# Performance work log

Hardware: AMD Instinct MI355X
Metric: run time of the kernel (lower is better)

The kernel has to match this reference:

```python
import jax, jax.numpy as jnp
import numpy as np

N = 100000   # total nodes
E = 1000000  # edges
D = 64       # input_dim
H = 128      # embed_dim


def setup_inputs() -> dict:
    key = jax.random.key(0)
    k1, k2, k3, k4 = jax.random.split(key, 4)
    nodes = jnp.arange(N, dtype=jnp.int32)
    features = jax.random.normal(k1, (N, D), dtype=jnp.float32)
    edge_index = jax.random.randint(k2, (2, E), 0, N, dtype=jnp.int32)
    # nn.Linear(2*D, H): weight [H, 2D], bias [H]
    W = jax.random.normal(k3, (H, 2 * D), dtype=jnp.float32) / np.sqrt(2 * D)
    b = jax.random.normal(k4, (H,), dtype=jnp.float32) * 0.01
    return {"nodes": nodes, "features": features, "edge_index": edge_index,
            "W": W, "b": b}


def reference(nodes, features, edge_index, W, b):
    src, dst = edge_index[0], edge_index[1]
    # gcn=False: neighbors are undirected (both src->dst and dst->src).
    # Mean aggregator over all neighbors (full-neighborhood mean).
    ones = jnp.ones((E,), dtype=features.dtype)
    neigh_sum = (jax.ops.segment_sum(features[dst], src, num_segments=N)
                 + jax.ops.segment_sum(features[src], dst, num_segments=N))
    deg = (jax.ops.segment_sum(ones, src, num_segments=N)
           + jax.ops.segment_sum(ones, dst, num_segments=N))
    neigh_mean = neigh_sum / jnp.maximum(deg, 1.0)[:, None]  # [N, D]
    self_feats = features[nodes]            # [B, D]
    neigh_feats = neigh_mean[nodes]         # [B, D]
    combined = jnp.concatenate([self_feats, neigh_feats], axis=1)  # [B, 2D]
    out = jax.nn.relu(combined @ W.T + b)   # [B, H]
    return out
```

## Files before the change

### kernel.cpp

```cpp
#include <hip/hip_runtime.h>
#include <hip/hip_bf16.h>


#define D_IN 64
#define H_OUT 128
#define CAP 64
#define CAP_L 61
#define NPB 32
#define BSHIFT 8
#define BUK_N 256
#define NBUK_MAX 512
#define PASSA_BLOCKS 256
#define PASSA_THREADS 512
#define OVF_CAP 32768

typedef unsigned long long ull;
typedef unsigned short ushortt;
typedef unsigned char uchar;
typedef __attribute__((ext_vector_type(8))) short bf16x8;
typedef __attribute__((ext_vector_type(4))) float f32x4;
typedef __attribute__((ext_vector_type(2))) float f32x2;

__device__ __forceinline__ ushortt f2bf(float f) {
    __hip_bfloat16 h = __float2bfloat16(f);
    return *reinterpret_cast<ushortt*>(&h);
}
__device__ __forceinline__ float bf2f(ushortt u) {
    unsigned int x = ((unsigned int)u) << 16;
    return __uint_as_float(x);
}

__global__ __launch_bounds__(PASSA_THREADS) void bucket_a_kernel(
    const int* __restrict__ ei,
    unsigned* __restrict__ gbuf,
    int* __restrict__ blkcnt,
    ull* __restrict__ ovf,
    int* __restrict__ ovfn,
    int E, int nbuk, int scap, int chunk)
{
    __shared__ int lcnt[NBUK_MAX];
    const int t = threadIdx.x;
    for (int i = t; i < nbuk; i += PASSA_THREADS) lcnt[i] = 0;
    __syncthreads();

    const int E2 = 2 * E;
    int lo = blockIdx.x * chunk;
    int hi = lo + chunk; if (hi > E2) hi = E2;

    for (int i = lo + t; i < hi; i += PASSA_THREADS) {
        int u = ei[i];
        int v = (i < E) ? ei[E + i] : ei[i - E];
        int b = u >> BSHIFT;
        unsigned pk = ((unsigned)v << BSHIFT) | (unsigned)(u & (BUK_N - 1));
        int p = atomicAdd(&lcnt[b], 1);
        if (p < scap) {
            gbuf[((size_t)blockIdx.x * nbuk + b) * scap + p] = pk;
        } else {
            int gp = atomicAdd(ovfn, 1);
            if (gp < OVF_CAP) ovf[gp] = ((ull)(unsigned)v << 32) | (unsigned)u;
        }
    }
    __syncthreads();
    for (int b = t; b < nbuk; b += PASSA_THREADS) {
        int c = lcnt[b];
        blkcnt[blockIdx.x * nbuk + b] = c < scap ? c : scap;
    }
}

__global__ __launch_bounds__(512) void adj_lds_kernel(
    const unsigned* __restrict__ gbuf,
    const int* __restrict__ blkcnt,
    const ull* __restrict__ ovf,
    const int* __restrict__ ovfn,
    int* __restrict__ cnt,
    int* __restrict__ adj,
    int N, int nbuk, int scap)
{
    __shared__ unsigned adj_l[BUK_N * CAP_L];
    __shared__ int cnt_l[BUK_N];
    __shared__ int scnt_l[PASSA_BLOCKS];

    const int b = blockIdx.x;
    const int t = threadIdx.x;

    if (t < BUK_N) cnt_l[t] = 0;
    if (t < PASSA_BLOCKS) scnt_l[t] = blkcnt[t * nbuk + b];
    __syncthreads();

    const int wv   = t >> 6;
    const int lane = t & 63;

    for (int seg = wv; seg < PASSA_BLOCKS; seg += 8) {
        int c = scnt_l[seg];
        const unsigned* base = gbuf + ((size_t)seg * nbuk + b) * scap;
        for (int i = lane; i < c; i += 64) {
            unsigned e = base[i];
            int ul = e & (BUK_N - 1);
            int v  = (int)(e >> BSHIFT);
            int p  = atomicAdd(&cnt_l[ul], 1);
            if (p < CAP_L) adj_l[ul * CAP_L + p] = (unsigned)v;
        }
    }
    __syncthreads();

    int novf = *ovfn; if (novf > OVF_CAP) novf = OVF_CAP;
    for (int i = t; i < novf; i += 512) {
        ull pk = ovf[i];
        int u = (int)(unsigned)(pk & 0xffffffffu);
        if ((u >> BSHIFT) == b) {
            int v = (int)(unsigned)(pk >> 32);
            int ul = u & (BUK_N - 1);
            int p  = atomicAdd(&cnt_l[ul], 1);
            if (p < CAP_L) adj_l[ul * CAP_L + p] = (unsigned)v;
        }
    }
    __syncthreads();

    if (t < BUK_N) {
        int g = (b << BSHIFT) + t;
        if (g < N) {
            int c = cnt_l[t];
            cnt[g] = c;
            int cl = c < CAP_L ? c : CAP_L;
            int k4 = (cl + 3) >> 2;
            for (int s = 0; s < k4; ++s) {
                uint4 o;
                o.x = adj_l[t * CAP_L + 4 * s + 0];
                o.y = adj_l[t * CAP_L + 4 * s + 1];
                o.z = adj_l[t * CAP_L + 4 * s + 2];
                o.w = adj_l[t * CAP_L + 4 * s + 3];
                *(uint4*)&adj[(size_t)g * CAP + 4 * s] = o;
            }
        }
    }
}

__global__ __launch_bounds__(256) void build_adj_kernel(
    const int* __restrict__ ei,
    int* __restrict__ cnt,
    int* __restrict__ adj,
    int E)
{
    const int part   = blockIdx.x & 7;
    const int bloc   = blockIdx.x >> 3;
    const int nbp    = gridDim.x >> 3;
    const int stride = nbp * 256;
    const int E2     = 2 * E;

    for (int i = bloc * 256 + (int)threadIdx.x; i < E2; i += stride) {
        int u = ei[i];
        if (((u >> 4) & 7) != part) continue;
        int v = (i < E) ? ei[E + i] : ei[i - E];
        int p = atomicAdd(&cnt[u], 1);
        if (p < CAP_L) adj[u * CAP + p] = v;
    }
}

__global__ __launch_bounds__(256) void convert_kernel(
    const float4* __restrict__ feat4,
    const float4* __restrict__ w4,
    ushortt* __restrict__ fb,
    uint2* __restrict__ fq,
    ushortt* __restrict__ Wb,
    int* __restrict__ ovfn,
    int nfeat8, int nw8)
{
    if (blockIdx.x == 0 && threadIdx.x == 0) *ovfn = 0;
    int i = blockIdx.x * 256 + threadIdx.x;
    if (i < nfeat8) {
        float4 a = feat4[2 * i], b = feat4[2 * i + 1];
        bf16x8 o;
        o[0] = (short)f2bf(a.x); o[1] = (short)f2bf(a.y);
        o[2] = (short)f2bf(a.z); o[3] = (short)f2bf(a.w);
        o[4] = (short)f2bf(b.x); o[5] = (short)f2bf(b.y);
        o[6] = (short)f2bf(b.z); o[7] = (short)f2bf(b.w);
        *(bf16x8*)&fb[(size_t)i * 8] = o;
        unsigned lo = (unsigned)__builtin_amdgcn_cvt_pk_fp8_f32(a.x, a.y, 0, false);
        lo = (unsigned)__builtin_amdgcn_cvt_pk_fp8_f32(a.z, a.w, (int)lo, true);
        unsigned hi = (unsigned)__builtin_amdgcn_cvt_pk_fp8_f32(b.x, b.y, 0, false);
        hi = (unsigned)__builtin_amdgcn_cvt_pk_fp8_f32(b.z, b.w, (int)hi, true);
        uint2 q; q.x = lo; q.y = hi;
        fq[i] = q;
    } else {
        int j = i - nfeat8;
        if (j < nw8) {
            float4 a = w4[2 * j], b = w4[2 * j + 1];
            bf16x8 o;
            o[0] = (short)f2bf(a.x); o[1] = (short)f2bf(a.y);
            o[2] = (short)f2bf(a.z); o[3] = (short)f2bf(a.w);
            o[4] = (short)f2bf(b.x); o[5] = (short)f2bf(b.y);
            o[6] = (short)f2bf(b.z); o[7] = (short)f2bf(b.w);
            *(bf16x8*)&Wb[(size_t)j * 8] = o;
        }
    }
}

__global__ __launch_bounds__(256) void aggregate_fp8_kernel(
    const uchar* __restrict__ fq,
    const int* __restrict__ adj,
    const int* __restrict__ cnt,
    ushortt* __restrict__ meanb,
    int N)
{
    int wid  = (blockIdx.x * blockDim.x + threadIdx.x) >> 6;
    int lane = threadIdx.x & 63;
    if (wid >= N) return;

    const int oct = lane >> 3;
    const int ol  = lane & 7;

    int c  = cnt[wid];
    int cc = c < CAP_L ? c : CAP_L;

    int ids = 0;
    if (lane < cc) ids = adj[wid * CAP + lane];

    f32x2 s0 = {0.f, 0.f}, s1 = {0.f, 0.f}, s2 = {0.f, 0.f}, s3 = {0.f, 0.f};

    int j = 0;
    for (; j + 8 < cc; j += 16) {
        int j0 = j + oct;
        int j1 = j + 8 + oct;
        int a1 = j1 < cc;
        int id0 = __shfl(ids, j0);
        int id1 = __shfl(ids, a1 ? j1 : cc - 1);
        uint2 u0 = *(const uint2*)(fq + (size_t)id0 * 64 + ol * 8);
        uint2 u1 = *(const uint2*)(fq + (size_t)id1 * 64 + ol * 8);
        if (!a1) { u1.x = 0u; u1.y = 0u; }
        s0 += __builtin_amdgcn_cvt_pk_f32_fp8((int)u0.x, false);
        s1 += __builtin_amdgcn_cvt_pk_f32_fp8((int)u0.x, true);
        s2 += __builtin_amdgcn_cvt_pk_f32_fp8((int)u0.y, false);
        s3 += __builtin_amdgcn_cvt_pk_f32_fp8((int)u0.y, true);
        s0 += __builtin_amdgcn_cvt_pk_f32_fp8((int)u1.x, false);
        s1 += __builtin_amdgcn_cvt_pk_f32_fp8((int)u1.x, true);
        s2 += __builtin_amdgcn_cvt_pk_f32_fp8((int)u1.y, false);
        s3 += __builtin_amdgcn_cvt_pk_f32_fp8((int)u1.y, true);
    }
    if (j < cc) {
        int j0 = j + oct;
        int a0 = j0 < cc;
        int id0 = __shfl(ids, a0 ? j0 : cc - 1);
        uint2 u0 = *(const uint2*)(fq + (size_t)id0 * 64 + ol * 8);
        if (!a0) { u0.x = 0u; u0.y = 0u; }
        s0 += __builtin_amdgcn_cvt_pk_f32_fp8((int)u0.x, false);
        s1 += __builtin_amdgcn_cvt_pk_f32_fp8((int)u0.x, true);
        s2 += __builtin_amdgcn_cvt_pk_f32_fp8((int)u0.y, false);
        s3 += __builtin_amdgcn_cvt_pk_f32_fp8((int)u0.y, true);
    }

#pragma unroll
    for (int m = 8; m <= 32; m <<= 1) {
        f32x2 t;
        t.x = __shfl_xor(s0.x, m); t.y = __shfl_xor(s0.y, m); s0 += t;
        t.x = __shfl_xor(s1.x, m); t.y = __shfl_xor(s1.y, m); s1 += t;
        t.x = __shfl_xor(s2.x, m); t.y = __shfl_xor(s2.y, m); s2 += t;
        t.x = __shfl_xor(s3.x, m); t.y = __shfl_xor(s3.y, m); s3 += t;
    }

    if (oct == 0) {
        float r = 1.0f / fmaxf((float)c, 1.0f);
        bf16x8 o;
        o[0] = (short)f2bf(s0.x * r); o[1] = (short)f2bf(s0.y * r);
        o[2] = (short)f2bf(s1.x * r); o[3] = (short)f2bf(s1.y * r);
        o[4] = (short)f2bf(s2.x * r); o[5] = (short)f2bf(s2.y * r);
        o[6] = (short)f2bf(s3.x * r); o[7] = (short)f2bf(s3.y * r);
        *(bf16x8*)&meanb[(size_t)wid * D_IN + ol * 8] = o;
    }
}

__global__ __launch_bounds__(256) void aggregate_f32_kernel(
    const float* __restrict__ feat,
    const int* __restrict__ adj,
    const int* __restrict__ cnt,
    ushortt* __restrict__ meanb,
    int N)
{
    int wid  = (blockIdx.x * blockDim.x + threadIdx.x) >> 6;
    int lane = threadIdx.x & 63;
    if (wid >= N) return;

    int c  = cnt[wid];
    int cc = c < CAP_L ? c : CAP_L;
    int ids = adj[wid * CAP + lane];

    float sum = 0.0f;
    int j = 0;
    for (; j + 8 <= cc; j += 8) {
        int i0 = __shfl(ids, j + 0);
        int i1 = __shfl(ids, j + 1);
        int i2 = __shfl(ids, j + 2);
        int i3 = __shfl(ids, j + 3);
        int i4 = __shfl(ids, j + 4);
        int i5 = __shfl(ids, j + 5);
        int i6 = __shfl(ids, j + 6);
        int i7 = __shfl(ids, j + 7);
        float f0 = feat[i0 * D_IN + lane];
        float f1 = feat[i1 * D_IN + lane];
        float f2 = feat[i2 * D_IN + lane];
        float f3 = feat[i3 * D_IN + lane];
        float f4 = feat[i4 * D_IN + lane];
        float f5 = feat[i5 * D_IN + lane];
        float f6 = feat[i6 * D_IN + lane];
        float f7 = feat[i7 * D_IN + lane];
        sum += ((f0 + f1) + (f2 + f3)) + ((f4 + f5) + (f6 + f7));
    }
    for (; j < cc; ++j)
        sum += feat[__shfl(ids, j) * D_IN + lane];

    float m = sum / fmaxf((float)c, 1.0f);
    meanb[(size_t)wid * D_IN + lane] = f2bf(m);
}

__global__ __launch_bounds__(256) void gemm_mfma_kernel(
    const int* __restrict__ nodes,
    const ushortt* __restrict__ fb,
    const ushortt* __restrict__ meanb,
    const ushortt* __restrict__ Wb,
    const float* __restrict__ bias,
    float* __restrict__ out,
    int N)
{
    __shared__ ushortt w_lds[128 * 136];
    __shared__ int gnode[64];

    const int t  = threadIdx.x;
    const int n0 = blockIdx.x * 64;

    if (t < 64) {
        int idx = n0 + t;
        gnode[t] = nodes[idx < N ? idx : N - 1];
    }
    for (int i = t; i < 128 * 16; i += 256) {
        int row = i >> 4, seg = i & 15;
        *(bf16x8*)&w_lds[row * 136 + seg * 8] =
            *(const bf16x8*)&Wb[row * 128 + seg * 8];
    }
    __syncthreads();

    const int w    = t >> 6;
    const int lane = t & 63;
    const int l15  = lane & 15;
    const int quad = lane >> 4;

    const int g = gnode[w * 16 + l15];
    const bf16x8 a0 = *(const bf16x8*)&fb[(size_t)g * D_IN +  0 + quad * 8];
    const bf16x8 a1 = *(const bf16x8*)&fb[(size_t)g * D_IN + 32 + quad * 8];
    const bf16x8 a2 = *(const bf16x8*)&meanb[(size_t)g * D_IN +  0 + quad * 8];
    const bf16x8 a3 = *(const bf16x8*)&meanb[(size_t)g * D_IN + 32 + quad * 8];

    const int  out_row = n0 + w * 16 + l15;
    const bool valid   = out_row < N;

#pragma unroll
    for (int tile = 0; tile < 8; ++tile) {
        const int h0 = tile * 16;
        const ushortt* wrow = &w_lds[(h0 + l15) * 136];
        bf16x8 b0 = *(const bf16x8*)&wrow[ 0 + quad * 8];
        bf16x8 b1 = *(const bf16x8*)&wrow[32 + quad * 8];
        bf16x8 b2 = *(const bf16x8*)&wrow[64 + quad * 8];
        bf16x8 b3 = *(const bf16x8*)&wrow[96 + quad * 8];

        f32x4 acc = {0.f, 0.f, 0.f, 0.f};
        acc = __builtin_amdgcn_mfma_f32_16x16x32_bf16(b0, a0, acc, 0, 0, 0);
        acc = __builtin_amdgcn_mfma_f32_16x16x32_bf16(b1, a1, acc, 0, 0, 0);
        acc = __builtin_amdgcn_mfma_f32_16x16x32_bf16(b2, a2, acc, 0, 0, 0);
        acc = __builtin_amdgcn_mfma_f32_16x16x32_bf16(b3, a3, acc, 0, 0, 0);

        if (valid) {
            float4 bv = *(const float4*)&bias[h0 + quad * 4];
            float4 o;
            o.x = fmaxf(acc[0] + bv.x, 0.0f);
            o.y = fmaxf(acc[1] + bv.y, 0.0f);
            o.z = fmaxf(acc[2] + bv.z, 0.0f);
            o.w = fmaxf(acc[3] + bv.w, 0.0f);
            *(float4*)&out[(size_t)out_row * H_OUT + h0 + quad * 4] = o;
        }
    }
}

__global__ __launch_bounds__(256) void gemm_kernel(
    const int* __restrict__ nodes,
    const float* __restrict__ feat,
    const ushortt* __restrict__ meanb,
    const float* __restrict__ W,
    const float* __restrict__ bias,
    float* __restrict__ out,
    int N)
{
    __shared__ float w_lds[64 * 132];
    __shared__ float comb_self[NPB * 68];
    __shared__ float comb_mean[NPB * 68];
    __shared__ int   gnode[NPB];

    const int t  = threadIdx.x;
    const int n0 = blockIdx.x * NPB;

    if (t < NPB) {
        int idx = n0 + t;
        if (idx >= N) idx = N - 1;
        gnode[t] = nodes[idx];
    }
    __syncthreads();

    for (int i = t; i < NPB * 64; i += 256) {
        int n = i >> 6, d = i & 63;
        int g = gnode[n];
        comb_self[n * 68 + d] = feat[g * D_IN + d];
        comb_mean[n * 68 + d] = bf2f(meanb[(size_t)g * D_IN + d]);
    }
    for (int i = t; i < H_OUT * 64; i += 256) {
        int h = i >> 6, kk = i & 63;
        w_lds[kk * 132 + h] = W[h * (2 * D_IN) + kk];
    }
    __syncthreads();

    const int tx = t & 31;
    const int ty = t >> 5;
    const int h0 = tx * 4;
    const int nl = ty * 4;

    float acc[4][4];
#pragma unroll
    for (int j = 0; j < 4; j++)
#pragma unroll
        for (int i = 0; i < 4; i++) acc[j][i] = 0.0f;

    for (int kk = 0; kk < 64; kk += 4) {
        float4 wvv[4], cv[4];
#pragma unroll
        for (int i = 0; i < 4; i++)
            wvv[i] = *(const float4*)&w_lds[(kk + i) * 132 + h0];
#pragma unroll
        for (int j = 0; j < 4; j++)
            cv[j] = *(const float4*)&comb_self[(nl + j) * 68 + kk];
#pragma unroll
        for (int j = 0; j < 4; j++) {
            const float* c = (const float*)&cv[j];
#pragma unroll
            for (int i = 0; i < 4; i++) {
                const float* wp = (const float*)&wvv[i];
                acc[j][0] += wp[0] * c[i];
                acc[j][1] += wp[1] * c[i];
                acc[j][2] += wp[2] * c[i];
                acc[j][3] += wp[3] * c[i];
            }
        }
    }
    __syncthreads();

    for (int i = t; i < H_OUT * 64; i += 256) {
        int h = i >> 6, kk = i & 63;
        w_lds[kk * 132 + h] = W[h * (2 * D_IN) + 64 + kk];
    }
    __syncthreads();

    for (int kk = 0; kk < 64; kk += 4) {
        float4 wvv[4], cv[4];
#pragma unroll
        for (int i = 0; i < 4; i++)
            wvv[i] = *(const float4*)&w_lds[(kk + i) * 132 + h0];
#pragma unroll
        for (int j = 0; j < 4; j++)
            cv[j] = *(const float4*)&comb_mean[(nl + j) * 68 + kk];
#pragma unroll
        for (int j = 0; j < 4; j++) {
            const float* c = (const float*)&cv[j];
#pragma unroll
            for (int i = 0; i < 4; i++) {
                const float* wp = (const float*)&wvv[i];
                acc[j][0] += wp[0] * c[i];
                acc[j][1] += wp[1] * c[i];
                acc[j][2] += wp[2] * c[i];
                acc[j][3] += wp[3] * c[i];
            }
        }
    }

    float4 bv = *(const float4*)&bias[h0];
#pragma unroll
    for (int j = 0; j < 4; j++) {
        int n = n0 + nl + j;
        if (n >= N) continue;
        float4 o;
        o.x = fmaxf(acc[j][0] + bv.x, 0.0f);
        o.y = fmaxf(acc[j][1] + bv.y, 0.0f);
        o.z = fmaxf(acc[j][2] + bv.z, 0.0f);
        o.w = fmaxf(acc[j][3] + bv.w, 0.0f);
        *(float4*)&out[(size_t)n * H_OUT + h0] = o;
    }
}

extern "C" void kernel_launch(void* const* d_in, const int* in_sizes, int n_in,
                              void* d_out, int out_size, void* d_ws, size_t ws_size,
                              hipStream_t stream) {
    const int*   nodes = (const int*)d_in[0];
    const float* feat  = (const float*)d_in[1];
    const int*   ei    = (const int*)d_in[2];
    const float* W     = (const float*)d_in[3];
    const float* bias  = (const float*)d_in[4];
    float*       out   = (float*)d_out;

    const int N  = in_sizes[0];
    const int E  = in_sizes[2] / 2;
    const int E2 = 2 * E;

    const int nbuk  = (N + BUK_N - 1) >> BSHIFT;
    const int chunk = (E2 + PASSA_BLOCKS - 1) / PASSA_BLOCKS;
    double ex = (double)chunk * (double)BUK_N / (double)N;
    int scap = ((int)(ex + 5.0 * __builtin_sqrt(ex)) + 31) & ~15;

    char* base = (char*)d_ws;
    size_t off = 0;
    auto aln = [](size_t x) { return (x + 63) & ~(size_t)63; };
    int*     cnt    = (int*)(base + off);     off = aln(off + (size_t)N * 4);
    int*     ovfn   = (int*)(base + off);     off = aln(off + 64);
    int*     adj    = (int*)(base + off);     off = aln(off + (size_t)N * CAP * 4);
    ushortt* meanb  = (ushortt*)(base + off); off = aln(off + (size_t)N * D_IN * 2);
    const size_t off_min = off;
    int*     blkcnt = (int*)(base + off);     off = aln(off + (size_t)PASSA_BLOCKS * NBUK_MAX * 4);
    ull*     ovf    = (ull*)(base + off);     off = aln(off + (size_t)OVF_CAP * 8);
    ushortt* Wb     = (ushortt*)(base + off); off = aln(off + (size_t)H_OUT * 2 * D_IN * 2);
    ushortt* fb     = (ushortt*)(base + off); off = aln(off + (size_t)N * D_IN * 2);
    uchar*   fq     = (uchar*)(base + off);   off = aln(off + (size_t)N * D_IN);
    unsigned* gbuf  = (unsigned*)(base + off);
    const size_t total = off + (size_t)PASSA_BLOCKS * nbuk * scap * 4;

    const bool full = (N <= 131072) && (nbuk <= NBUK_MAX) && (ws_size >= total)
                   && ((N * D_IN) % 8 == 0);

    const int ablocks = (int)(((size_t)N * 64 + 255) / 256);

    if (full) {
        const int nfeat8 = N * D_IN / 8;
        const int nw8    = H_OUT * 2 * D_IN / 8;
        convert_kernel<<<(nfeat8 + nw8 + 255) / 256, 256, 0, stream>>>(
            (const float4*)feat, (const float4*)W, fb, (uint2*)fq, Wb, ovfn,
            nfeat8, nw8);
        bucket_a_kernel<<<PASSA_BLOCKS, PASSA_THREADS, 0, stream>>>(
            ei, gbuf, blkcnt, ovf, ovfn, E, nbuk, scap, chunk);
        adj_lds_kernel<<<nbuk, 512, 0, stream>>>(gbuf, blkcnt, ovf, ovfn,
                                                 cnt, adj, N, nbuk, scap);
        aggregate_fp8_kernel<<<ablocks, 256, 0, stream>>>(fq, adj, cnt,
                                                          meanb, N);
        gemm_mfma_kernel<<<(N + 63) / 64, 256, 0, stream>>>(
            nodes, fb, meanb, Wb, bias, out, N);
    } else {
        (void)off_min;
        hipMemsetAsync(cnt, 0, (size_t)N * sizeof(int), stream);
        build_adj_kernel<<<2048, 256, 0, stream>>>(ei, cnt, adj, E);
        aggregate_f32_kernel<<<ablocks, 256, 0, stream>>>(feat, adj, cnt,
                                                          meanb, N);
        gemm_kernel<<<(N + NPB - 1) / NPB, 256, 0, stream>>>(
            nodes, feat, meanb, W, bias, out, N);
    }
}
```

Before: 192.9 us.

## Fuse convert into bucketing pass, drop overflow list, unroll fp8 aggregation

Merges the feature/weight conversion kernel into the edge-bucketing kernel as extra blocks, which removes one launch and lets the two independent jobs run concurrently. The global overflow list and its atomic counter are removed. Instead, segment capacity is enlarged, and any bucket whose segment overflowed falls back to rescanning the full edge list. The fp8 neighbor aggregation now issues up to four gathers up front for the first 32 neighbors, and replaces the butterfly reduction with a transpose-style reduction in which each lane writes one output element. The trade-offs are a larger gbuf footprint and a very slow fallback path if a segment ever saturates.

Result: no change. 196.7 us (+2.0%).

```diff
diff --git a/kernel.cpp b/kernel.cpp
--- a/kernel.cpp
+++ b/kernel.cpp
@@ -12,7 +12,6 @@
 #define NBUK_MAX 512
 #define PASSA_BLOCKS 256
 #define PASSA_THREADS 512
-#define OVF_CAP 32768
 
 typedef unsigned long long ull;
 typedef unsigned short ushortt;
@@ -30,16 +29,51 @@
     return __uint_as_float(x);
 }
 
-__global__ __launch_bounds__(PASSA_THREADS) void bucket_a_kernel(
+__global__ __launch_bounds__(PASSA_THREADS) void prep_kernel(
     const int* __restrict__ ei,
     unsigned* __restrict__ gbuf,
     int* __restrict__ blkcnt,
-    ull* __restrict__ ovf,
-    int* __restrict__ ovfn,
-    int E, int nbuk, int scap, int chunk)
-{
+    const float4* __restrict__ feat4,
+    const float4* __restrict__ w4,
+    ushortt* __restrict__ fb,
+    uint2* __restrict__ fq,
+    ushortt* __restrict__ Wb,
+    int E, int nbuk, int scap, int chunk, int nfeat8, int nw8)
+{
+    const int t = threadIdx.x;
+
+    if (blockIdx.x >= PASSA_BLOCKS) {
+        int i = (blockIdx.x - PASSA_BLOCKS) * PASSA_THREADS + t;
+        if (i < nfeat8) {
+            float4 a = feat4[2 * i], b = feat4[2 * i + 1];
+            bf16x8 o;
+            o[0] = (short)f2bf(a.x); o[1] = (short)f2bf(a.y);
+            o[2] = (short)f2bf(a.z); o[3] = (short)f2bf(a.w);
+            o[4] = (short)f2bf(b.x); o[5] = (short)f2bf(b.y);
+            o[6] = (short)f2bf(b.z); o[7] = (short)f2bf(b.w);
+            *(bf16x8*)&fb[(size_t)i * 8] = o;
+            unsigned lo = (unsigned)__builtin_amdgcn_cvt_pk_fp8_f32(a.x, a.y, 0, false);
+            lo = (unsigned)__builtin_amdgcn_cvt_pk_fp8_f32(a.z, a.w, (int)lo, true);
+            unsigned hi = (unsigned)__builtin_amdgcn_cvt_pk_fp8_f32(b.x, b.y, 0, false);
+            hi = (unsigned)__builtin_amdgcn_cvt_pk_fp8_f32(b.z, b.w, (int)hi, true);
+            uint2 q; q.x = lo; q.y = hi;
+            fq[i] = q;
+        } else {
+            int j = i - nfeat8;
+            if (j < nw8) {
+                float4 a = w4[2 * j], b = w4[2 * j + 1];
+                bf16x8 o;
+                o[0] = (short)f2bf(a.x); o[1] = (short)f2bf(a.y);
+                o[2] = (short)f2bf(a.z); o[3] = (short)f2bf(a.w);
+                o[4] = (short)f2bf(b.x); o[5] = (short)f2bf(b.y);
+                o[6] = (short)f2bf(b.z); o[7] = (short)f2bf(b.w);
+                *(bf16x8*)&Wb[(size_t)j * 8] = o;
+            }
+        }
+        return;
+    }
+
     __shared__ int lcnt[NBUK_MAX];
-    const int t = threadIdx.x;
     for (int i = t; i < nbuk; i += PASSA_THREADS) lcnt[i] = 0;
     __syncthreads();
 
@@ -53,65 +87,61 @@
         int b = u >> BSHIFT;
         unsigned pk = ((unsigned)v << BSHIFT) | (unsigned)(u & (BUK_N - 1));
         int p = atomicAdd(&lcnt[b], 1);
-        if (p < scap) {
-            gbuf[((size_t)blockIdx.x * nbuk + b) * scap + p] = pk;
-        } else {
-            int gp = atomicAdd(ovfn, 1);
-            if (gp < OVF_CAP) ovf[gp] = ((ull)(unsigned)v << 32) | (unsigned)u;
-        }
-    }
-    __syncthreads();
-    for (int b = t; b < nbuk; b += PASSA_THREADS) {
-        int c = lcnt[b];
-        blkcnt[blockIdx.x * nbuk + b] = c < scap ? c : scap;
-    }
+        if (p < scap) gbuf[((size_t)blockIdx.x * nbuk + b) * scap + p] = pk;
+    }
+    __syncthreads();
+    for (int b = t; b < nbuk; b += PASSA_THREADS)
+        blkcnt[blockIdx.x * nbuk + b] = lcnt[b];
 }
 
 __global__ __launch_bounds__(512) void adj_lds_kernel(
     const unsigned* __restrict__ gbuf,
     const int* __restrict__ blkcnt,
-    const ull* __restrict__ ovf,
-    const int* __restrict__ ovfn,
+    const int* __restrict__ ei,
     int* __restrict__ cnt,
     int* __restrict__ adj,
-    int N, int nbuk, int scap)
+    int N, int E, int nbuk, int scap)
 {
     __shared__ unsigned adj_l[BUK_N * CAP_L];
     __shared__ int cnt_l[BUK_N];
     __shared__ int scnt_l[PASSA_BLOCKS];
+    __shared__ int satf;
 
     const int b = blockIdx.x;
     const int t = threadIdx.x;
 
+    if (t == 0) satf = 0;
     if (t < BUK_N) cnt_l[t] = 0;
-    if (t < PASSA_BLOCKS) scnt_l[t] = blkcnt[t * nbuk + b];
-    __syncthreads();
-
-    const int wv   = t >> 6;
-    const int lane = t & 63;
-
-    for (int seg = wv; seg < PASSA_BLOCKS; seg += 8) {
-        int c = scnt_l[seg];
-        const unsigned* base = gbuf + ((size_t)seg * nbuk + b) * scap;
-        for (int i = lane; i < c; i += 64) {
-            unsigned e = base[i];
-            int ul = e & (BUK_N - 1);
-            int v  = (int)(e >> BSHIFT);
-            int p  = atomicAdd(&cnt_l[ul], 1);
-            if (p < CAP_L) adj_l[ul * CAP_L + p] = (unsigned)v;
-        }
-    }
-    __syncthreads();
-
-    int novf = *ovfn; if (novf > OVF_CAP) novf = OVF_CAP;
-    for (int i = t; i < novf; i += 512) {
-        ull pk = ovf[i];
-        int u = (int)(unsigned)(pk & 0xffffffffu);
-        if ((u >> BSHIFT) == b) {
-            int v = (int)(unsigned)(pk >> 32);
+    if (t < PASSA_BLOCKS) {
+        int c = blkcnt[t * nbuk + b];
+        scnt_l[t] = c;
+        if (c > scap) satf = 1;
+    }
+    __syncthreads();
+
+    if (satf) {
+        const int E2 = 2 * E;
+        for (int i = t; i < E2; i += 512) {
+            int u = ei[i];
+            if ((u >> BSHIFT) != b) continue;
+            int v = (i < E) ? ei[E + i] : ei[i - E];
             int ul = u & (BUK_N - 1);
             int p  = atomicAdd(&cnt_l[ul], 1);
             if (p < CAP_L) adj_l[ul * CAP_L + p] = (unsigned)v;
+        }
+    } else {
+        const int wv   = t >> 6;
+        const int lane = t & 63;
+        for (int seg = wv; seg < PASSA_BLOCKS; seg += 8) {
+            int c = scnt_l[seg]; if (c > scap) c = scap;
+            const unsigned* base = gbuf + ((size_t)seg * nbuk + b) * scap;
+            for (int i = lane; i < c; i += 64) {
+                unsigned e = base[i];
+                int ul = e & (BUK_N - 1);
+                int v  = (int)(e >> BSHIFT);
+                int p  = atomicAdd(&cnt_l[ul], 1);
+                if (p < CAP_L) adj_l[ul * CAP_L + p] = (unsigned)v;
+            }
         }
     }
     __syncthreads();
@@ -156,45 +186,6 @@
     }
 }
 
-__global__ __launch_bounds__(256) void convert_kernel(
-    const float4* __restrict__ feat4,
-    const float4* __restrict__ w4,
-    ushortt* __restrict__ fb,
-    uint2* __restrict__ fq,
-    ushortt* __restrict__ Wb,
-    int* __restrict__ ovfn,
-    int nfeat8, int nw8)
-{
-    if (blockIdx.x == 0 && threadIdx.x == 0) *ovfn = 0;
-    int i = blockIdx.x * 256 + threadIdx.x;
-    if (i < nfeat8) {
-        float4 a = feat4[2 * i], b = feat4[2 * i + 1];
-        bf16x8 o;
-        o[0] = (short)f2bf(a.x); o[1] = (short)f2bf(a.y);
-        o[2] = (short)f2bf(a.z); o[3] = (short)f2bf(a.w);
-        o[4] = (short)f2bf(b.x); o[5] = (short)f2bf(b.y);
-        o[6] = (short)f2bf(b.z); o[7] = (short)f2bf(b.w);
-        *(bf16x8*)&fb[(size_t)i * 8] = o;
-        unsigned lo = (unsigned)__builtin_amdgcn_cvt_pk_fp8_f32(a.x, a.y, 0, false);
-        lo = (unsigned)__builtin_amdgcn_cvt_pk_fp8_f32(a.z, a.w, (int)lo, true);
-        unsigned hi = (unsigned)__builtin_amdgcn_cvt_pk_fp8_f32(b.x, b.y, 0, false);
-        hi = (unsigned)__builtin_amdgcn_cvt_pk_fp8_f32(b.z, b.w, (int)hi, true);
-        uint2 q; q.x = lo; q.y = hi;
-        fq[i] = q;
-    } else {
-        int j = i - nfeat8;
-        if (j < nw8) {
-            float4 a = w4[2 * j], b = w4[2 * j + 1];
-            bf16x8 o;
-            o[0] = (short)f2bf(a.x); o[1] = (short)f2bf(a.y);
-            o[2] = (short)f2bf(a.z); o[3] = (short)f2bf(a.w);
-            o[4] = (short)f2bf(b.x); o[5] = (short)f2bf(b.y);
-            o[6] = (short)f2bf(b.z); o[7] = (short)f2bf(b.w);
-            *(bf16x8*)&Wb[(size_t)j * 8] = o;
-        }
-    }
-}
-
 __global__ __launch_bounds__(256) void aggregate_fp8_kernel(
     const uchar* __restrict__ fq,
     const int* __restrict__ adj,
@@ -209,63 +200,86 @@
     const int oct = lane >> 3;
     const int ol  = lane & 7;
 
-    int c  = cnt[wid];
+    int c = cnt[wid];
+    int ids = 0;
+    if (lane < 32) ids = adj[wid * CAP + lane];
+
     int cc = c < CAP_L ? c : CAP_L;
-
-    int ids = 0;
-    if (lane < cc) ids = adj[wid * CAP + lane];
+    if (__builtin_expect(cc > 32, 0)) {
+        if (lane >= 32 && lane < cc) ids = adj[wid * CAP + lane];
+    }
+
+    const uchar* fqb = fq + ol * 8;
+
+    uint2 u0 = {0u, 0u}, u1 = {0u, 0u}, u2 = {0u, 0u}, u3 = {0u, 0u};
+    if (cc > 0) {
+        int jj = oct;      int a = jj < cc; int id = __shfl(ids, a ? jj : 0);
+        u0 = *(const uint2*)(fqb + (size_t)id * 64);
+        if (!a) { u0.x = 0u; u0.y = 0u; }
+    }
+    if (cc > 8) {
+        int jj = 8 + oct;  int a = jj < cc; int id = __shfl(ids, a ? jj : 0);
+        u1 = *(const uint2*)(fqb + (size_t)id * 64);
+        if (!a) { u1.x = 0u; u1.y = 0u; }
+    }
+    if (cc > 16) {
+        int jj = 16 + oct; int a = jj < cc; int id = __shfl(ids, a ? jj : 0);
+        u2 = *(const uint2*)(fqb + (size_t)id * 64);
+        if (!a) { u2.x = 0u; u2.y = 0u; }
+    }
+    if (cc > 24) {
+        int jj = 24 + oct; int a = jj < cc; int id = __shfl(ids, a ? jj : 0);
+        u3 = *(const uint2*)(fqb + (size_t)id * 64);
+        if (!a) { u3.x = 0u; u3.y = 0u; }
+    }
 
     f32x2 s0 = {0.f, 0.f}, s1 = {0.f, 0.f}, s2 = {0.f, 0.f}, s3 = {0.f, 0.f};
-
-    int j = 0;
-    for (; j + 8 < cc; j += 16) {
-        int j0 = j + oct;
-        int j1 = j + 8 + oct;
-        int a1 = j1 < cc;
-        int id0 = __shfl(ids, j0);
-        int id1 = __shfl(ids, a1 ? j1 : cc - 1);
-        uint2 u0 = *(const uint2*)(fq + (size_t)id0 * 64 + ol * 8);
-        uint2 u1 = *(const uint2*)(fq + (size_t)id1 * 64 + ol * 8);
-        if (!a1) { u1.x = 0u; u1.y = 0u; }
-        s0 += __builtin_amdgcn_cvt_pk_f32_fp8((int)u0.x, false);
-        s1 += __builtin_amdgcn_cvt_pk_f32_fp8((int)u0.x, true);
-        s2 += __builtin_amdgcn_cvt_pk_f32_fp8((int)u0.y, false);
-        s3 += __builtin_amdgcn_cvt_pk_f32_fp8((int)u0.y, true);
-        s0 += __builtin_amdgcn_cvt_pk_f32_fp8((int)u1.x, false);
-        s1 += __builtin_amdgcn_cvt_pk_f32_fp8((int)u1.x, true);
-        s2 += __builtin_amdgcn_cvt_pk_f32_fp8((int)u1.y, false);
-        s3 += __builtin_amdgcn_cvt_pk_f32_fp8((int)u1.y, true);
-    }
-    if (j < cc) {
-        int j0 = j + oct;
-        int a0 = j0 < cc;
-        int id0 = __shfl(ids, a0 ? j0 : cc - 1);
-        uint2 u0 = *(const uint2*)(fq + (size_t)id0 * 64 + ol * 8);
-        if (!a0) { u0.x = 0u; u0.y = 0u; }
-        s0 += __builtin_amdgcn_cvt_pk_f32_fp8((int)u0.x, false);
-        s1 += __builtin_amdgcn_cvt_pk_f32_fp8((int)u0.x, true);
-        s2 += __builtin_amdgcn_cvt_pk_f32_fp8((int)u0.y, false);
-        s3 += __builtin_amdgcn_cvt_pk_f32_fp8((int)u0.y, true);
-    }
-
-#pragma unroll
-    for (int m = 8; m <= 32; m <<= 1) {
-        f32x2 t;
-        t.x = __shfl_xor(s0.x, m); t.y = __shfl_xor(s0.y, m); s0 += t;
-        t.x = __shfl_xor(s1.x, m); t.y = __shfl_xor(s1.y, m); s1 += t;
-        t.x = __shfl_xor(s2.x, m); t.y = __shfl_xor(s2.y, m); s2 += t;
-        t.x = __shfl_xor(s3.x, m); t.y = __shfl_xor(s3.y, m); s3 += t;
-    }
-
-    if (oct == 0) {
-        float r = 1.0f / fmaxf((float)c, 1.0f);
-        bf16x8 o;
-        o[0] = (short)f2bf(s0.x * r); o[1] = (short)f2bf(s0.y * r);
-        o[2] = (short)f2bf(s1.x * r); o[3] = (short)f2bf(s1.y * r);
-        o[4] = (short)f2bf(s2.x * r); o[5] = (short)f2bf(s2.y * r);
-        o[6] = (short)f2bf(s3.x * r); o[7] = (short)f2bf(s3.y * r);
-        *(bf16x8*)&meanb[(size_t)wid * D_IN + ol * 8] = o;
-    }
+#define DEC(u)                                                       \
+    s0 += __builtin_amdgcn_cvt_pk_f32_fp8((int)(u).x, false);        \
+    s1 += __builtin_amdgcn_cvt_pk_f32_fp8((int)(u).x, true);         \
+    s2 += __builtin_amdgcn_cvt_pk_f32_fp8((int)(u).y, false);        \
+    s3 += __builtin_amdgcn_cvt_pk_f32_fp8((int)(u).y, true);
+    DEC(u0); DEC(u1); DEC(u2); DEC(u3);
+
+    if (__builtin_expect(cc > 32, 0)) {
+        for (int j = 32; j < cc; j += 8) {
+            int jj = j + oct; int a = jj < cc; int id = __shfl(ids, a ? jj : 0);
+            uint2 u = *(const uint2*)(fqb + (size_t)id * 64);
+            if (!a) { u.x = 0u; u.y = 0u; }
+            DEC(u);
+        }
+    }
+#undef DEC
+
+    f32x2 a0, a1;
+    {
+        f32x2 t0, t1, t2, t3;
+        t0.x = __shfl_xor(s0.x, 8);  t0.y = __shfl_xor(s0.y, 8);
+        t1.x = __shfl_xor(s1.x, 8);  t1.y = __shfl_xor(s1.y, 8);
+        t2.x = __shfl_xor(s2.x, 8);  t2.y = __shfl_xor(s2.y, 8);
+        t3.x = __shfl_xor(s3.x, 8);  t3.y = __shfl_xor(s3.y, 8);
+        bool hi = (oct & 1);
+        a0 = hi ? (s2 + t2) : (s0 + t0);
+        a1 = hi ? (s3 + t3) : (s1 + t1);
+    }
+    f32x2 b0;
+    {
+        f32x2 t0, t1;
+        t0.x = __shfl_xor(a0.x, 16); t0.y = __shfl_xor(a0.y, 16);
+        t1.x = __shfl_xor(a1.x, 16); t1.y = __shfl_xor(a1.y, 16);
+        bool hi = (oct & 2);
+        b0 = hi ? (a1 + t1) : (a0 + t0);
+    }
+    float cf;
+    {
+        f32x2 tt; tt.x = __shfl_xor(b0.x, 32); tt.y = __shfl_xor(b0.y, 32);
+        f32x2 ss = b0 + tt;
+        cf = (oct & 4) ? ss.y : ss.x;
+    }
+
+    float r = 1.0f / fmaxf((float)c, 1.0f);
+    int d = 8 * ol + 4 * (oct & 1) + (oct & 2) + ((oct >> 2) & 1);
+    meanb[(size_t)wid * D_IN + d] = f2bf(cf * r);
 }
 
 __global__ __launch_bounds__(256) void aggregate_f32_kernel(
@@ -507,18 +521,16 @@
     const int nbuk  = (N + BUK_N - 1) >> BSHIFT;
     const int chunk = (E2 + PASSA_BLOCKS - 1) / PASSA_BLOCKS;
     double ex = (double)chunk * (double)BUK_N / (double)N;
-    int scap = ((int)(ex + 5.0 * __builtin_sqrt(ex)) + 31) & ~15;
+    int scap = ((int)(ex + 9.0 * __builtin_sqrt(ex)) + 31) & ~15;
+    if (scap < 64) scap = 64;
 
     char* base = (char*)d_ws;
     size_t off = 0;
     auto aln = [](size_t x) { return (x + 63) & ~(size_t)63; };
     int*     cnt    = (int*)(base + off);     off = aln(off + (size_t)N * 4);
-    int*     ovfn   = (int*)(base + off);     off = aln(off + 64);
     int*     adj    = (int*)(base + off);     off = aln(off + (size_t)N * CAP * 4);
     ushortt* meanb  = (ushortt*)(base + off); off = aln(off + (size_t)N * D_IN * 2);
-    const size_t off_min = off;
     int*     blkcnt = (int*)(base + off);     off = aln(off + (size_t)PASSA_BLOCKS * NBUK_MAX * 4);
-    ull*     ovf    = (ull*)(base + off);     off = aln(off + (size_t)OVF_CAP * 8);
     ushortt* Wb     = (ushortt*)(base + off); off = aln(off + (size_t)H_OUT * 2 * D_IN * 2);
     ushortt* fb     = (ushortt*)(base + off); off = aln(off + (size_t)N * D_IN * 2);
     uchar*   fq     = (uchar*)(base + off);   off = aln(off + (size_t)N * D_IN);
@@ -533,19 +545,17 @@
     if (full) {
         const int nfeat8 = N * D_IN / 8;
         const int nw8    = H_OUT * 2 * D_IN / 8;
-        convert_kernel<<<(nfeat8 + nw8 + 255) / 256, 256, 0, stream>>>(
-            (const float4*)feat, (const float4*)W, fb, (uint2*)fq, Wb, ovfn,
-            nfeat8, nw8);
-        bucket_a_kernel<<<PASSA_BLOCKS, PASSA_THREADS, 0, stream>>>(
-            ei, gbuf, blkcnt, ovf, ovfn, E, nbuk, scap, chunk);
-        adj_lds_kernel<<<nbuk, 512, 0, stream>>>(gbuf, blkcnt, ovf, ovfn,
-                                                 cnt, adj, N, nbuk, scap);
+        const int conv_blocks = (nfeat8 + nw8 + PASSA_THREADS - 1) / PASSA_THREADS;
+        prep_kernel<<<PASSA_BLOCKS + conv_blocks, PASSA_THREADS, 0, stream>>>(
+            ei, gbuf, blkcnt, (const float4*)feat, (const float4*)W,
+            fb, (uint2*)fq, Wb, E, nbuk, scap, chunk, nfeat8, nw8);
+        adj_lds_kernel<<<nbuk, 512, 0, stream>>>(gbuf, blkcnt, ei,
+                                                 cnt, adj, N, E, nbuk, scap);
         aggregate_fp8_kernel<<<ablocks, 256, 0, stream>>>(fq, adj, cnt,
                                                           meanb, N);
         gemm_mfma_kernel<<<(N + 63) / 64, 256, 0, stream>>>(
             nodes, fb, meanb, Wb, bias, out, N);
     } else {
-        (void)off_min;
         hipMemsetAsync(cnt, 0, (size_t)N * sizeof(int), stream);
         build_adj_kernel<<<2048, 256, 0, stream>>>(ei, cnt, adj, E);
         aggregate_f32_kernel<<<ablocks, 256, 0, stream>>>(feat, adj, cnt,
```
